# Performance work log

Measured on AMD Instinct MI355X. Metric: run time of the kernel, lower is better.

Reference implementation:

```python
import jax, jax.numpy as jnp
import numpy as np

N = 8192
F_IN = 256
F_OUT = 64
ALPHA = 0.2  # LeakyReLU negative slope
MASK_VAL = -9e15


def setup_inputs() -> dict:
    key = jax.random.key(0)
    k1, k2, k3, k4 = jax.random.split(key, 4)
    h = jax.random.normal(k1, (N, F_IN), dtype=jnp.float32)
    adj = jax.random.randint(k2, (N, N), 0, 2, dtype=jnp.int32)  # 0/1 dense adjacency
    # Parameters (original creates them inside forward with xavier init; here fixed inputs)
    W = jax.random.normal(k3, (F_IN, F_OUT), dtype=jnp.float32) * (1.414 * np.sqrt(2.0 / (F_IN + F_OUT)))
    a = jax.random.normal(k4, (2 * F_OUT, 1), dtype=jnp.float32) * (1.414 * np.sqrt(2.0 / (2 * F_OUT + 1)))
    return {"h": h, "adj": adj, "W": W, "a": a}


def reference(h, adj, W, a):
    # Wh: [N, F_OUT]
    Wh = h @ W
    # e_ij = LeakyReLU(a^T [Wh_i ; Wh_j]) computed via broadcast instead of the
    f_src = Wh @ a[:F_OUT, 0]   # [N] contribution of row node i
    f_dst = Wh @ a[F_OUT:, 0]   # [N] contribution of col node j
    e = jax.nn.leaky_relu(f_src[:, None] + f_dst[None, :], negative_slope=ALPHA)  # [N, N]
    # adj-masked row softmax
    scores = jnp.where(adj > 0, e, MASK_VAL)
    attention = jax.nn.softmax(scores, axis=1)
    # dropout omitted (deterministic eval reference)
    h_prime = attention @ Wh  # [N, F_OUT]
    return jax.nn.elu(h_prime)  # concat=True branch
```

## Files before the change

kernel.cpp:

```cpp
#include <hip/hip_runtime.h>
#include <hip/hip_bf16.h>

#define NN 8192
#define FIN 256
#define FOUT 64
#define L2E 1.4426950408889634f
#define PADK 40

typedef __attribute__((ext_vector_type(8))) short short8;
typedef __attribute__((ext_vector_type(4))) float f32x4;
typedef __attribute__((ext_vector_type(4))) int   iv4;

#define BAR() do { \
  __asm__ __volatile__("s_waitcnt lgkmcnt(0)" ::: "memory"); \
  __builtin_amdgcn_s_barrier(); \
  __asm__ __volatile__("" ::: "memory"); \
} while (0)

__device__ __forceinline__ unsigned short f2bf(float x){
  unsigned u = __float_as_uint(x);
  u += 0x7FFFu + ((u >> 16) & 1u);
  return (unsigned short)(u >> 16);
}

__device__ __forceinline__ unsigned spread4(unsigned x){
  x &= 0xFFu;
  x = (x | (x << 12)) & 0x000F000Fu;
  x = (x | (x << 6))  & 0x03030303u;
  x = (x | (x << 3))  & 0x11111111u;
  return x;
}

__device__ __forceinline__ void cv_process(iv4 d, int l,
                                           unsigned* __restrict__ mp, int g){
  unsigned n = (unsigned)(d.x != 0)        | ((unsigned)(d.y != 0) << 1)
             | ((unsigned)(d.z != 0) << 2) | ((unsigned)(d.w != 0) << 3);
  unsigned long long B0 = __ballot((n & 1u) != 0);
  unsigned long long B1 = __ballot((n & 2u) != 0);
  unsigned long long B2 = __ballot((n & 4u) != 0);
  unsigned long long B3 = __ballot((n & 8u) != 0);
  const int hi = l & 4, sh = (l & 3) * 8;
  unsigned b0 = (unsigned)((hi ? (B0 >> 32) : B0) >> sh);
  unsigned b1 = (unsigned)((hi ? (B1 >> 32) : B1) >> sh);
  unsigned b2 = (unsigned)((hi ? (B2 >> 32) : B2) >> sh);
  unsigned b3 = (unsigned)((hi ? (B3 >> 32) : B3) >> sh);
  unsigned word = spread4(b0) | (spread4(b1) << 1)
                | (spread4(b2) << 2) | (spread4(b3) << 3);
  if (l < 8) mp[g*8 + l] = word;
}

__global__ __launch_bounds__(256) void k_pm(const float* __restrict__ h,
    const float* __restrict__ W, const float* __restrict__ a,
    const int* __restrict__ adj, unsigned short* __restrict__ WhT,
    float* __restrict__ fs, float* __restrict__ fd,
    unsigned* __restrict__ gmax_u, unsigned* __restrict__ mask){
  const int bid = blockIdx.x, t = threadIdx.x;
  const int l = t & 63, wv = t >> 6;
  if (bid % 3 == 0){
    const int pid = bid / 3;
    __shared__ float Ws[128*64];
    __shared__ float hs[8][128];
    const int rb = pid * 8;
    float acc0 = 0.f, acc1 = 0.f;
    for (int half = 0; half < 2; ++half){
      if (half) __syncthreads();
      for (int i = t; i < 2048; i += 256)
        ((float4*)Ws)[i] = ((const float4*)W)[half*2048 + i];
      {
        int rr = t >> 5, cc = t & 31;
        ((float4*)&hs[rr][0])[cc] =
            *(const float4*)(h + (size_t)(rb+rr)*FIN + half*128 + cc*4);
      }
      __syncthreads();
      #pragma unroll 8
      for (int k = 0; k < 128; ++k){
        float wval = Ws[k*64 + l];
        acc0 = fmaf(hs[wv*2+0][k], wval, acc0);
        acc1 = fmaf(hs[wv*2+1][k], wval, acc1);
      }
    }
    const int r0 = rb + wv*2, r1 = r0 + 1;
    float a1 = a[l], a2 = a[64 + l];
    float p0 = acc0*a1, q0 = acc0*a2, p1 = acc1*a1, q1 = acc1*a2;
    #pragma unroll
    for (int m = 1; m < 64; m <<= 1){
      p0 += __shfl_xor(p0, m); q0 += __shfl_xor(q0, m);
      p1 += __shfl_xor(p1, m); q1 += __shfl_xor(q1, m);
    }
    if (l == 0){
      fs[r0] = p0*L2E; fs[r1] = p1*L2E; fd[r0] = q0*L2E; fd[r1] = q1*L2E;
      atomicMax(gmax_u, __float_as_uint(q0*L2E + 64.0f));
      atomicMax(gmax_u, __float_as_uint(q1*L2E + 64.0f));
    }
    WhT[(size_t)l*NN + r0] = f2bf(acc0);
    WhT[(size_t)l*NN + r1] = f2bf(acc1);
  } else {
    const int cid = bid - bid/3 - 1;
    const unsigned rowid = (unsigned)cid*4u + (unsigned)wv;
    const iv4* __restrict__ ap = (const iv4*)(adj + (size_t)rowid*8192u) + l;
    unsigned* __restrict__ mp = mask + rowid*256u;
    iv4 d0 = ap[0*64], d1 = ap[1*64], d2 = ap[2*64], d3 = ap[3*64];
    iv4 d4 = ap[4*64], d5 = ap[5*64], d6 = ap[6*64], d7 = ap[7*64];
    #pragma unroll 1
    for (int i = 0; i < 32; i += 8){
      cv_process(d0, l, mp, i+0); if (i+ 8 < 32) d0 = ap[(i+ 8)*64];
      cv_process(d1, l, mp, i+1); if (i+ 9 < 32) d1 = ap[(i+ 9)*64];
      cv_process(d2, l, mp, i+2); if (i+10 < 32) d2 = ap[(i+10)*64];
      cv_process(d3, l, mp, i+3); if (i+11 < 32) d3 = ap[(i+11)*64];
      cv_process(d4, l, mp, i+4); if (i+12 < 32) d4 = ap[(i+12)*64];
      cv_process(d5, l, mp, i+5); if (i+13 < 32) d5 = ap[(i+13)*64];
      cv_process(d6, l, mp, i+6); if (i+14 < 32) d6 = ap[(i+14)*64];
      cv_process(d7, l, mp, i+7); if (i+15 < 32) d7 = ap[(i+15)*64];
    }
  }
}

__device__ __forceinline__ void attn_math(unsigned mbits, f32x4 fv0, f32x4 fv1,
    short8 w0, short8 w1, short8 w2, short8 w3,
    float fsrL, float mL, f32x4* acc, float& s0, float& s1){
  const float fv[8] = {fv0[0],fv0[1],fv0[2],fv0[3], fv1[0],fv1[1],fv1[2],fv1[3]};
  float w[8];
  #pragma unroll
  for (int j = 0; j < 8; ++j){
    float x  = fsrL + fv[j];
    float tt = fmaxf(x, 0.2f*x);
    float e  = __builtin_amdgcn_exp2f(tt - mL);
    w[j] = (mbits & (1u << j)) ? e : 0.0f;
  }
  s0 += (w[0]+w[2]) + (w[4]+w[6]);
  s1 += (w[1]+w[3]) + (w[5]+w[7]);
  short8 af;
  __hip_bfloat162* afp = (__hip_bfloat162*)&af;
  #pragma unroll
  for (int j = 0; j < 4; ++j)
    afp[j] = __float22bfloat162_rn(make_float2(w[2*j], w[2*j+1]));
  acc[0] = __builtin_amdgcn_mfma_f32_16x16x32_bf16(af, w0, acc[0], 0,0,0);
  acc[1] = __builtin_amdgcn_mfma_f32_16x16x32_bf16(af, w1, acc[1], 0,0,0);
  acc[2] = __builtin_amdgcn_mfma_f32_16x16x32_bf16(af, w2, acc[2], 0,0,0);
  acc[3] = __builtin_amdgcn_mfma_f32_16x16x32_bf16(af, w3, acc[3], 0,0,0);
}

__global__ __launch_bounds__(256, 4) void k_attn(const unsigned* __restrict__ mask,
    const unsigned short* __restrict__ WhT, const float* __restrict__ fs,
    const float* __restrict__ fd, const unsigned* __restrict__ gmax_u,
    float* __restrict__ acc_out, float* __restrict__ s_out){
  __shared__ unsigned short bslab[2][64*PADK];
  __shared__ float fslab[2][32];
  const int t = threadIdx.x, l = t & 63, wv = t >> 6;
  const int g = blockIdx.x & 127;
  const int kchunk = blockIdx.x >> 7;
  const int row = l & 15, quad = l >> 4;
  const int ibase = g*64 + wv*16;
  const int irow  = ibase + row;
  const float gmaxL = __uint_as_float(*gmax_u) - 64.0f;
  const float fsrL  = fs[irow];
  const float xL    = fsrL + gmaxL;
  const float mL    = fmaxf(xL, 0.2f*xL);

  const unsigned jbase = (unsigned)kchunk*1024u;
  const unsigned m_off = (unsigned)irow*256u + (jbase >> 5);
  const unsigned sg_off = (unsigned)l*8192u + jbase + (unsigned)wv*8u;
  const int      sl_off = l*PADK + wv*8;
  const int      qsh    = quad*8;

  f32x4 acc[4];
  #pragma unroll
  for (int nb = 0; nb < 4; ++nb) acc[nb] = (f32x4){0.f,0.f,0.f,0.f};

  {
    short8 v = *(const short8*)(WhT + sg_off);
    *(short8*)&bslab[0][sl_off] = v;
    if (t < 32) fslab[0][t] = fd[jbase + t];
  }
  unsigned m0 = mask[m_off + 0] >> qsh;
  unsigned m1 = mask[m_off + 1] >> qsh;

  float s0 = 0.f, s1 = 0.f;
  short8 nw; float nf = 0.f;

  #pragma unroll 1
  for (int s = 0; s < 32; s += 2){
    BAR();
    nw = *(const short8*)(WhT + sg_off + (s+1)*32);
    if (t < 32) nf = fd[jbase + (s+1)*32 + t];
    {
      f32x4 fv0 = *(const f32x4*)&fslab[0][qsh];
      f32x4 fv1 = *(const f32x4*)&fslab[0][qsh + 4];
      short8 w0 = *(const short8*)&bslab[0][( 0 + row)*PADK + qsh];
      short8 w1 = *(const short8*)&bslab[0][(16 + row)*PADK + qsh];
      short8 w2 = *(const short8*)&bslab[0][(32 + row)*PADK + qsh];
      short8 w3 = *(const short8*)&bslab[0][(48 + row)*PADK + qsh];
      attn_math(m0, fv0, fv1, w0, w1, w2, w3, fsrL, mL, acc, s0, s1);
    }
    if (s + 2 < 32) m0 = mask[m_off + s + 2] >> qsh;
    *(short8*)&bslab[1][sl_off] = nw;
    if (t < 32) fslab[1][t] = nf;

    BAR();
    if (s + 2 < 32){
      nw = *(const short8*)(WhT + sg_off + (s+2)*32);
      if (t < 32) nf = fd[jbase + (s+2)*32 + t];
    }
    {
      f32x4 fv0 = *(const f32x4*)&fslab[1][qsh];
      f32x4 fv1 = *(const f32x4*)&fslab[1][qsh + 4];
      short8 w0 = *(const short8*)&bslab[1][( 0 + row)*PADK + qsh];
      short8 w1 = *(const short8*)&bslab[1][(16 + row)*PADK + qsh];
      short8 w2 = *(const short8*)&bslab[1][(32 + row)*PADK + qsh];
      short8 w3 = *(const short8*)&bslab[1][(48 + row)*PADK + qsh];
      attn_math(m1, fv0, fv1, w0, w1, w2, w3, fsrL, mL, acc, s0, s1);
    }
    if (s + 3 < 32) m1 = mask[m_off + s + 3] >> qsh;
    if (s + 2 < 32){
      *(short8*)&bslab[0][sl_off] = nw;
      if (t < 32) fslab[0][t] = nf;
    }
  }

  float sacc = s0 + s1;
  sacc += __shfl_xor(sacc, 16);
  sacc += __shfl_xor(sacc, 32);
  if (l < 16) s_out[kchunk*NN + ibase + l] = sacc;
  float* op = acc_out + ((size_t)kchunk*NN + ibase)*FOUT;
  #pragma unroll
  for (int nb = 0; nb < 4; ++nb)
    #pragma unroll
    for (int r = 0; r < 4; ++r)
      op[(quad*4 + r)*FOUT + nb*16 + row] = acc[nb][r];
}

__global__ __launch_bounds__(256) void k_out(const float* __restrict__ acc,
    const float* __restrict__ s, float* __restrict__ out){
  const int idx = blockIdx.x*256 + threadIdx.x;
  const int i = idx >> 6;
  float num = 0.f, den = 0.f;
  #pragma unroll
  for (int ks = 0; ks < 8; ++ks){
    num += acc[idx + (size_t)ks*(NN*FOUT)];
    den += s[i + ks*NN];
  }
  float x = num / den;
  out[idx] = (x > 0.f) ? x : (__expf(x) - 1.0f);
}

extern "C" void kernel_launch(void* const* d_in, const int* in_sizes, int n_in,
                              void* d_out, int out_size, void* d_ws, size_t ws_size,
                              hipStream_t stream){
  const float* h   = (const float*)d_in[0];
  const int*   adj = (const int*)d_in[1];
  const float* W   = (const float*)d_in[2];
  const float* a   = (const float*)d_in[3];
  char* ws = (char*)d_ws;
  unsigned short* WhT = (unsigned short*)ws;
  float*    fs     = (float*)(ws + (1u<<20));
  float*    fd     = (float*)(ws + (1u<<20) + 32768);
  unsigned* gmax_u = (unsigned*)(ws + (1u<<20) + 65536);
  float*    acc    = (float*)(ws + (2u<<20));
  float*    s_ws   = (float*)(ws + (20u<<20));
  unsigned* mask   = (unsigned*)(ws + (48u<<20));

  (void)hipMemsetAsync(gmax_u, 0, 4, stream);
  k_pm<<<3072, 256, 0, stream>>>(h, W, a, adj, WhT, fs, fd, gmax_u, mask);
  k_attn<<<1024, 256, 0, stream>>>(mask, WhT, fs, fd, gmax_u, acc, s_ws);
  k_out<<<2048, 256, 0, stream>>>(acc, s_ws, (float*)d_out);
}
```

Baseline: 444.6 us.

## Restructure adjacency bit-packing blocks to grid-stride quarter-row chunks with double-buffered loads

```diff
diff --git a/kernel.cpp b/kernel.cpp
--- a/kernel.cpp
+++ b/kernel.cpp
@@ -56,8 +56,8 @@
     unsigned* __restrict__ gmax_u, unsigned* __restrict__ mask){
   const int bid = blockIdx.x, t = threadIdx.x;
   const int l = t & 63, wv = t >> 6;
-  if (bid % 3 == 0){
-    const int pid = bid / 3;
+  if ((bid & 1) == 0){
+    const int pid = bid >> 1;
     __shared__ float Ws[128*64];
     __shared__ float hs[8][128];
     const int rb = pid * 8;
@@ -95,22 +95,23 @@
     WhT[(size_t)l*NN + r0] = f2bf(acc0);
     WhT[(size_t)l*NN + r1] = f2bf(acc1);
   } else {
-    const int cid = bid - bid/3 - 1;
-    const unsigned rowid = (unsigned)cid*4u + (unsigned)wv;
-    const iv4* __restrict__ ap = (const iv4*)(adj + (size_t)rowid*8192u) + l;
-    unsigned* __restrict__ mp = mask + rowid*256u;
-    iv4 d0 = ap[0*64], d1 = ap[1*64], d2 = ap[2*64], d3 = ap[3*64];
-    iv4 d4 = ap[4*64], d5 = ap[5*64], d6 = ap[6*64], d7 = ap[7*64];
+    const unsigned cid = (unsigned)(bid >> 1);
+    const iv4* __restrict__ base = (const iv4*)adj;
+    const unsigned wvo = (unsigned)wv*128u + (unsigned)l;
+    unsigned s0q = cid, s1q = cid + 1024u;
+    iv4 d0 = base[s0q*512u + wvo], d1 = base[s0q*512u + wvo + 64u];
+    iv4 e0 = base[s1q*512u + wvo], e1 = base[s1q*512u + wvo + 64u];
     #pragma unroll 1
-    for (int i = 0; i < 32; i += 8){
-      cv_process(d0, l, mp, i+0); if (i+ 8 < 32) d0 = ap[(i+ 8)*64];
-      cv_process(d1, l, mp, i+1); if (i+ 9 < 32) d1 = ap[(i+ 9)*64];
-      cv_process(d2, l, mp, i+2); if (i+10 < 32) d2 = ap[(i+10)*64];
-      cv_process(d3, l, mp, i+3); if (i+11 < 32) d3 = ap[(i+11)*64];
-      cv_process(d4, l, mp, i+4); if (i+12 < 32) d4 = ap[(i+12)*64];
-      cv_process(d5, l, mp, i+5); if (i+13 < 32) d5 = ap[(i+13)*64];
-      cv_process(d6, l, mp, i+6); if (i+14 < 32) d6 = ap[(i+14)*64];
-      cv_process(d7, l, mp, i+7); if (i+15 < 32) d7 = ap[(i+15)*64];
+    for (int it = 0; it < 32; ++it){
+      const unsigned cur = cid + (unsigned)it*1024u;
+      unsigned nx2 = cur + 2048u; if (nx2 > 32767u) nx2 = 32767u;
+      iv4 f0 = base[nx2*512u + wvo], f1 = base[nx2*512u + wvo + 64u];
+      const unsigned row = cur >> 2, q = cur & 3u;
+      unsigned* __restrict__ mp = mask + row*256u;
+      const int g0 = (int)(q*8u) + 2*wv;
+      cv_process(d0, l, mp, g0);
+      cv_process(d1, l, mp, g0 + 1);
+      d0 = e0; d1 = e1; e0 = f0; e1 = f1;
     }
   }
 }
@@ -260,7 +261,7 @@
   unsigned* mask   = (unsigned*)(ws + (48u<<20));
 
   (void)hipMemsetAsync(gmax_u, 0, 4, stream);
-  k_pm<<<3072, 256, 0, stream>>>(h, W, a, adj, WhT, fs, fd, gmax_u, mask);
+  k_pm<<<2048, 256, 0, stream>>>(h, W, a, adj, WhT, fs, fd, gmax_u, mask);
   k_attn<<<1024, 256, 0, stream>>>(mask, WhT, fs, fd, gmax_u, acc, s_ws);
   k_out<<<2048, 256, 0, stream>>>(acc, s_ws, (float*)d_out);
 }
```

New measurement: 468.7 us. +5.4%, slower.
